# Kernel tuning notes

Measured on AMD Instinct MI355X. Metric: run time of the kernel, lower is better.

The kernel has to match this reference:

```python
import jax, jax.numpy as jnp
import numpy as np

N = 50000
E = 800000
H = 4
D = 64
NEG_SLOPE = 0.2


def gat_conv(h, W, al, ar, b, src, dst):
    # DGL GATConv (eval mode, no dropout): Wh = h @ W -> [N,H,D]
    Wh = (h @ W).reshape(N, H, D)
    el = jnp.sum(Wh * al[None], axis=-1)  # [N,H]
    er = jnp.sum(Wh * ar[None], axis=-1)  # [N,H]
    e = el[src] + er[dst]                 # [E,H]
    e = jnp.where(e > 0, e, NEG_SLOPE * e)  # leaky_relu
    # edge softmax per destination node
    m = jax.lax.stop_gradient(jax.ops.segment_max(e, dst, num_segments=N))
    m = jnp.where(jnp.isfinite(m), m, 0.0)
    ex = jnp.exp(e - m[dst])              # [E,H]
    s = jax.ops.segment_sum(ex, dst, num_segments=N)
    alpha = ex / s[dst]                   # [E,H]
    msg = Wh[src] * alpha[:, :, None]     # [E,H,D]
    out = jax.ops.segment_sum(msg, dst, num_segments=N)  # [N,H,D]
    out = out + b.reshape(1, H, D)
    out = jax.nn.elu(out)                 # activation=F.elu
    return out.reshape(N, H * D)


def setup_inputs() -> dict:
    key = jax.random.key(0)
    ks = jax.random.split(key, 16)
    inp = {
        "h": jax.random.normal(ks[0], (N, 256), dtype=jnp.float32),
        "src0": jax.random.randint(ks[1], (E,), 0, N, dtype=jnp.int32),
        "dst0": jax.random.randint(ks[2], (E,), 0, N, dtype=jnp.int32),
        "src1": jax.random.randint(ks[3], (E,), 0, N, dtype=jnp.int32),
        "dst1": jax.random.randint(ks[4], (E,), 0, N, dtype=jnp.int32),
        "W0": jax.random.normal(ks[5], (256, H * D), dtype=jnp.float32) * 0.05,
        "al0": jax.random.normal(ks[6], (H, D), dtype=jnp.float32) * 0.05,
        "ar0": jax.random.normal(ks[7], (H, D), dtype=jnp.float32) * 0.05,
        "b0": jnp.zeros((H * D,), dtype=jnp.float32),
        "W1": jax.random.normal(ks[8], (256, H * D), dtype=jnp.float32) * 0.05,
        "al1": jax.random.normal(ks[9], (H, D), dtype=jnp.float32) * 0.05,
        "ar1": jax.random.normal(ks[10], (H, D), dtype=jnp.float32) * 0.05,
        "b1": jnp.zeros((H * D,), dtype=jnp.float32),
        "Wp1": jax.random.normal(ks[11], (H * D, 128), dtype=jnp.float32) * 0.05,
        "bp1": jnp.zeros((128,), dtype=jnp.float32),
        "Wp2": jax.random.normal(ks[12], (128, 1), dtype=jnp.float32) * 0.05,
    }
    return inp


def reference(h, src0, dst0, src1, dst1, W0, al0, ar0, b0, W1, al1, ar1, b1, Wp1, bp1, Wp2):
    z0 = gat_conv(h, W0, al0, ar0, b0, src0, dst0)  # [N, H*D]
    z1 = gat_conv(h, W1, al1, ar1, b1, src1, dst1)  # [N, H*D]
    z = jnp.stack([z0, z1], axis=1)                 # [N, P=2, H*D]
    # SemanticAttention: Linear -> tanh -> Linear(no bias) -> softmax over meta-paths
    w = jnp.tanh(z @ Wp1 + bp1) @ Wp2               # [N, P, 1]
    beta = jax.nn.softmax(w[..., 0], axis=1)        # [N, P]
    return jnp.sum(beta[:, :, None] * z, axis=1)    # [N, H*D]
```

## Files before the change

kernel.cpp:

```cpp
#include <hip/hip_runtime.h>
#include <math.h>

#define NN 50000
#define NE 800000
#define NH 4
#define ND 64
#define NF 256
#define NEG_SLOPE 0.2f

typedef __attribute__((ext_vector_type(8))) short s16x8;
typedef __attribute__((ext_vector_type(4))) float f32x4;

__device__ __forceinline__ float elu1(float x) { return x > 0.f ? x : (__expf(x) - 1.f); }
__device__ __forceinline__ float lrelu(float x) { return x > 0.f ? x : NEG_SLOPE * x; }

__device__ __forceinline__ unsigned short f2b(float x) {
    unsigned int u = __float_as_uint(x);
    u = (u + 0x7FFFu + ((u >> 16) & 1u)) >> 16;
    return (unsigned short)u;
}
__device__ __forceinline__ float blo(unsigned int u) { return __uint_as_float(u << 16); }
__device__ __forceinline__ float bhi(unsigned int u) { return __uint_as_float(u & 0xFFFF0000u); }
__device__ __forceinline__ float sel4(float a0, float a1, float a2, float a3, int h) {
    float r = a0;
    r = (h == 1) ? a1 : r;
    r = (h == 2) ? a2 : r;
    r = (h == 3) ? a3 : r;
    return r;
}

__global__ __launch_bounds__(256) void prep(const float* __restrict__ W0,
                                            const float* __restrict__ W1,
                                            const float* __restrict__ Wp1,
                                            short* __restrict__ WT0,
                                            short* __restrict__ WT1,
                                            short* __restrict__ Wp1T) {
    int t = threadIdx.x, b = blockIdx.x, job = blockIdx.y;
    if (job < 2) {
        const float* W = job ? W1 : W0;
        short* WT = job ? WT1 : WT0;
        WT[b * 256 + t] = (short)f2b(W[t * 256 + b]);
    } else if (b < 128) {
        Wp1T[b * 256 + t] = (short)f2b(Wp1[t * 128 + b]);
    }
}

__global__ __launch_bounds__(256) void gemm_mfma(const float* __restrict__ A,
                                                 const short* __restrict__ WTb,
                                                 const float* __restrict__ al,
                                                 const float* __restrict__ ar,
                                                 unsigned short* __restrict__ Whb,
                                                 float* __restrict__ el,
                                                 float* __restrict__ er) {
    int t = threadIdx.x;
    int hh = t >> 6;
    int l = t & 63;
    int r16 = l & 15, kq = l >> 4;
    int m0 = blockIdx.x * 16;

    f32x4 acc[4] = {{0,0,0,0},{0,0,0,0},{0,0,0,0},{0,0,0,0}};
    const float* arow = A + (size_t)(m0 + r16) * 256;
    const short* bbase = WTb + (size_t)hh * 64 * 256;

    #pragma unroll
    for (int k0 = 0; k0 < 256; k0 += 32) {
        float4 f0 = *(const float4*)(arow + k0 + kq * 8);
        float4 f1 = *(const float4*)(arow + k0 + kq * 8 + 4);
        s16x8 af;
        af[0] = (short)f2b(f0.x); af[1] = (short)f2b(f0.y);
        af[2] = (short)f2b(f0.z); af[3] = (short)f2b(f0.w);
        af[4] = (short)f2b(f1.x); af[5] = (short)f2b(f1.y);
        af[6] = (short)f2b(f1.z); af[7] = (short)f2b(f1.w);
        #pragma unroll
        for (int nt = 0; nt < 4; ++nt) {
            s16x8 bf = *(const s16x8*)(bbase + (size_t)(nt * 16 + r16) * 256 + k0 + kq * 8);
            acc[nt] = __builtin_amdgcn_mfma_f32_16x16x32_bf16(af, bf, acc[nt], 0, 0, 0);
        }
    }

    float elp[4] = {0,0,0,0}, erp[4] = {0,0,0,0};
    #pragma unroll
    for (int nt = 0; nt < 4; ++nt) {
        int col = nt * 16 + r16;
        float alv = al[hh * 64 + col];
        float arv = ar[hh * 64 + col];
        #pragma unroll
        for (int r = 0; r < 4; ++r) {
            float v = acc[nt][r];
            int row = m0 + kq * 4 + r;
            Whb[(size_t)row * 256 + hh * 64 + col] = f2b(v);
            elp[r] += v * alv;
            erp[r] += v * arv;
        }
    }
    #pragma unroll
    for (int msk = 1; msk < 16; msk <<= 1) {
        #pragma unroll
        for (int r = 0; r < 4; ++r) {
            elp[r] += __shfl_xor(elp[r], msk);
            erp[r] += __shfl_xor(erp[r], msk);
        }
    }
    if (r16 == 0) {
        #pragma unroll
        for (int r = 0; r < 4; ++r) {
            int row = m0 + kq * 4 + r;
            el[row * 4 + hh] = elp[r];
            er[row * 4 + hh] = erp[r];
        }
    }
}

__global__ __launch_bounds__(256) void hist_kernel(const int* __restrict__ dst, int* __restrict__ deg) {
    int e = blockIdx.x * 256 + threadIdx.x;
    if (e < NE) atomicAdd(&deg[dst[e]], 1);
}

__global__ __launch_bounds__(256) void scan_blk(const int* __restrict__ deg,
                                                int* __restrict__ rp,
                                                int* __restrict__ bsum) {
    __shared__ int ls[256];
    int b = blockIdx.x, t = threadIdx.x;
    int base = b * 1024 + t * 4;
    int v0 = (base + 0 < NN) ? deg[base + 0] : 0;
    int v1 = (base + 1 < NN) ? deg[base + 1] : 0;
    int v2 = (base + 2 < NN) ? deg[base + 2] : 0;
    int v3 = (base + 3 < NN) ? deg[base + 3] : 0;
    int p0 = v0, p1 = p0 + v1, p2 = p1 + v2, p3 = p2 + v3;
    ls[t] = p3;
    __syncthreads();
    int x = p3;
    #pragma unroll
    for (int off = 1; off < 256; off <<= 1) {
        int add = (t >= off) ? ls[t - off] : 0;
        __syncthreads();
        x += add;
        ls[t] = x;
        __syncthreads();
    }
    int excl = x - p3;
    if (base + 0 < NN) rp[base + 0] = excl;
    if (base + 1 < NN) rp[base + 1] = excl + p0;
    if (base + 2 < NN) rp[base + 2] = excl + p1;
    if (base + 3 < NN) rp[base + 3] = excl + p2;
    if (t == 255) bsum[b] = x;
}

__global__ __launch_bounds__(64) void scan_tops(int* __restrict__ bsum, int* __restrict__ rp, int nblk) {
    int t = threadIdx.x;
    int orig = (t < nblk) ? bsum[t] : 0;
    int v = orig;
    #pragma unroll
    for (int off = 1; off < 64; off <<= 1) {
        int y = __shfl_up(v, off);
        if (t >= off) v += y;
    }
    bsum[t] = v - orig;
    int total = __shfl(v, nblk - 1);
    if (t == 0) rp[NN] = total;
}

__global__ __launch_bounds__(256) void scan_add(int* __restrict__ rp,
                                                const int* __restrict__ bsum,
                                                int* __restrict__ cur) {
    int i = blockIdx.x * 256 + threadIdx.x;
    if (i < NN) {
        int v = rp[i] + bsum[i >> 10];
        rp[i] = v;
        cur[i] = v;
    }
}

__global__ __launch_bounds__(256) void fill_kernel(const int* __restrict__ src,
                                                   const int* __restrict__ dst,
                                                   int* __restrict__ cur,
                                                   int* __restrict__ colv) {
    int e = blockIdx.x * 256 + threadIdx.x;
    if (e < NE) {
        int pos = atomicAdd(&cur[dst[e]], 1);
        colv[pos] = src[e];
    }
}

__global__ __launch_bounds__(512) void node_agg(const int* __restrict__ rp,
                                                const int* __restrict__ colv,
                                                const float* __restrict__ el,
                                                const float* __restrict__ er,
                                                const unsigned short* __restrict__ Whb,
                                                const float* __restrict__ bias,
                                                unsigned short* __restrict__ zb,
                                                int path) {
    int t = threadIdx.x;
    int wid = t >> 6;
    int lane = t & 63;
    int n = blockIdx.x * 8 + wid;
    int beg = rp[n], end = rp[n + 1];
    float4 erv = *(const float4*)&er[(size_t)n * 4];

    int eg = lane >> 4, sl = lane & 15;
    int h = sl >> 2;
    float er_h = sel4(erv.x, erv.y, erv.z, erv.w, h);
    float acc[16];
    #pragma unroll
    for (int i = 0; i < 16; ++i) acc[i] = 0.f;
    float s = 0.f;

    for (int j0 = beg; j0 < end; j0 += 4) {
        int j = j0 + eg;
        bool act = j < end;
        int sidx = colv[act ? j : beg];
        float e_l = el[(size_t)sidx * 4 + h];
        float p = act ? __expf(lrelu(e_l + er_h)) : 0.f;
        s += p;
        const unsigned short* wr = &Whb[(size_t)sidx * 256 + sl * 16];
        uint4 u0 = *(const uint4*)wr;
        uint4 u1 = *(const uint4*)(wr + 8);
        acc[0]  += p * blo(u0.x); acc[1]  += p * bhi(u0.x);
        acc[2]  += p * blo(u0.y); acc[3]  += p * bhi(u0.y);
        acc[4]  += p * blo(u0.z); acc[5]  += p * bhi(u0.z);
        acc[6]  += p * blo(u0.w); acc[7]  += p * bhi(u0.w);
        acc[8]  += p * blo(u1.x); acc[9]  += p * bhi(u1.x);
        acc[10] += p * blo(u1.y); acc[11] += p * bhi(u1.y);
        acc[12] += p * blo(u1.z); acc[13] += p * bhi(u1.z);
        acc[14] += p * blo(u1.w); acc[15] += p * bhi(u1.w);
    }
    #pragma unroll
    for (int i = 0; i < 16; ++i) {
        acc[i] += __shfl_xor(acc[i], 16);
        acc[i] += __shfl_xor(acc[i], 32);
    }
    s += __shfl_xor(s, 16);
    s += __shfl_xor(s, 32);

    if (lane < 16) {
        float inv = (s > 0.f) ? 1.f / s : 0.f;
        unsigned int pk[8];
        #pragma unroll
        for (int i = 0; i < 8; ++i) {
            float za = elu1(acc[2 * i] * inv + bias[sl * 16 + 2 * i]);
            float zbv = elu1(acc[2 * i + 1] * inv + bias[sl * 16 + 2 * i + 1]);
            pk[i] = (unsigned int)f2b(za) | ((unsigned int)f2b(zbv) << 16);
        }
        unsigned int* op = (unsigned int*)(zb + (size_t)n * 512 + path * 256 + sl * 16);
        uint4 o0 = {pk[0], pk[1], pk[2], pk[3]};
        uint4 o1 = {pk[4], pk[5], pk[6], pk[7]};
        *(uint4*)op = o0;
        *(uint4*)(op + 4) = o1;
    }
}

__global__ __launch_bounds__(256) void semantic_mfma(const unsigned short* __restrict__ zb,
                                                     const short* __restrict__ Wp1T,
                                                     const float* __restrict__ bp1,
                                                     const float* __restrict__ Wp2,
                                                     float* __restrict__ w) {
    int t = threadIdx.x;
    int gw = blockIdx.x * 4 + (t >> 6);
    if (gw >= 6250) return;
    int l = t & 63;
    int r16 = l & 15, kq = l >> 4;
    int row0 = gw * 16;
    int path = (row0 >= NN) ? 1 : 0;
    int rbase = path ? row0 - NN : row0;
    const unsigned short* arow = zb + (size_t)(rbase + r16) * 512 + path * 256;

    f32x4 acc[8] = {{0,0,0,0},{0,0,0,0},{0,0,0,0},{0,0,0,0},
                    {0,0,0,0},{0,0,0,0},{0,0,0,0},{0,0,0,0}};
    #pragma unroll
    for (int k0 = 0; k0 < 256; k0 += 32) {
        s16x8 af = *(const s16x8*)(arow + k0 + kq * 8);
        #pragma unroll
        for (int nt = 0; nt < 8; ++nt) {
            s16x8 bf = *(const s16x8*)(Wp1T + (size_t)(nt * 16 + r16) * 256 + k0 + kq * 8);
            acc[nt] = __builtin_amdgcn_mfma_f32_16x16x32_bf16(af, bf, acc[nt], 0, 0, 0);
        }
    }
    float wpart[4] = {0,0,0,0};
    #pragma unroll
    for (int nt = 0; nt < 8; ++nt) {
        int col = nt * 16 + r16;
        float bpv = bp1[col], wpv = Wp2[col];
        #pragma unroll
        for (int r = 0; r < 4; ++r) wpart[r] += tanhf(acc[nt][r] + bpv) * wpv;
    }
    #pragma unroll
    for (int msk = 1; msk < 16; msk <<= 1) {
        #pragma unroll
        for (int r = 0; r < 4; ++r) wpart[r] += __shfl_xor(wpart[r], msk);
    }
    if (r16 == 0) {
        #pragma unroll
        for (int r = 0; r < 4; ++r) w[row0 + kq * 4 + r] = wpart[r];
    }
}

__global__ __launch_bounds__(256) void combine(float* __restrict__ zio,
                                               const float* __restrict__ w) {
    int n = blockIdx.x * 4 + (threadIdx.x >> 6);
    int c = (threadIdx.x & 63) * 4;
    const unsigned short* z0p = (const unsigned short*)zio + (size_t)n * 512 + c;
    uint2 u0 = *(const uint2*)z0p;
    uint2 u1 = *(const uint2*)(z0p + 256);
    float w0v = w[n], w1v = w[n + NN];
    __syncthreads();
    float mw = fmaxf(w0v, w1v);
    float e0 = __expf(w0v - mw), e1 = __expf(w1v - mw);
    float inv = 1.f / (e0 + e1);
    float b0 = e0 * inv, b1 = e1 * inv;
    float4 o;
    o.x = b0 * blo(u0.x) + b1 * blo(u1.x);
    o.y = b0 * bhi(u0.x) + b1 * bhi(u1.x);
    o.z = b0 * blo(u0.y) + b1 * blo(u1.y);
    o.w = b0 * bhi(u0.y) + b1 * bhi(u1.y);
    *(float4*)&zio[(size_t)n * 256 + c] = o;
}

extern "C" void kernel_launch(void* const* d_in, const int* in_sizes, int n_in,
                              void* d_out, int out_size, void* d_ws, size_t ws_size,
                              hipStream_t stream) {
    const float* h   = (const float*)d_in[0];
    const int* src0  = (const int*)d_in[1];
    const int* dst0  = (const int*)d_in[2];
    const int* src1  = (const int*)d_in[3];
    const int* dst1  = (const int*)d_in[4];
    const float* W0  = (const float*)d_in[5];
    const float* al0 = (const float*)d_in[6];
    const float* ar0 = (const float*)d_in[7];
    const float* b0  = (const float*)d_in[8];
    const float* W1  = (const float*)d_in[9];
    const float* al1 = (const float*)d_in[10];
    const float* ar1 = (const float*)d_in[11];
    const float* b1  = (const float*)d_in[12];
    const float* Wp1 = (const float*)d_in[13];
    const float* bp1 = (const float*)d_in[14];
    const float* Wp2 = (const float*)d_in[15];

    unsigned short* Whb = (unsigned short*)d_ws;
    float* el  = (float*)(Whb + (size_t)NN * NF);
    float* er  = el + (size_t)NN * NH;
    float* w   = er + (size_t)NN * NH;
    int*   deg = (int*)(w + 2 * NN);
    int*   rp  = deg + NN;
    int*   cur = rp + NN + 1;
    int*   colv = cur + NN;
    int*   bsum = colv + NE;
    short* WT0 = (short*)(bsum + 64);
    short* WT1 = WT0 + 256 * 256;
    short* Wp1T = WT1 + 256 * 256;
    unsigned short* zb = (unsigned short*)d_out;

    const int NBLK = (NN + 1023) / 1024;

    prep<<<dim3(256, 3), 256, 0, stream>>>(W0, W1, Wp1, WT0, WT1, Wp1T);

    for (int p = 0; p < 2; ++p) {
        const int* src  = p ? src1 : src0;
        const int* dst  = p ? dst1 : dst0;
        const float* al = p ? al1 : al0;
        const float* ar = p ? ar1 : ar0;
        const float* bb = p ? b1 : b0;
        const short* WT = p ? WT1 : WT0;

        hipMemsetAsync(deg, 0, NN * sizeof(int), stream);
        hist_kernel<<<(NE + 255) / 256, 256, 0, stream>>>(dst, deg);
        scan_blk<<<NBLK, 256, 0, stream>>>(deg, rp, bsum);
        scan_tops<<<1, 64, 0, stream>>>(bsum, rp, NBLK);
        scan_add<<<(NN + 255) / 256, 256, 0, stream>>>(rp, bsum, cur);
        fill_kernel<<<(NE + 255) / 256, 256, 0, stream>>>(src, dst, cur, colv);
        gemm_mfma<<<NN / 16, 256, 0, stream>>>(h, WT, al, ar, Whb, el, er);
        node_agg<<<NN / 8, 512, 0, stream>>>(rp, colv, el, er, Whb, bb, zb, p);
    }
    semantic_mfma<<<(6250 + 3) / 4, 256, 0, stream>>>(zb, Wp1T, bp1, Wp2, w);
    combine<<<NN / 4, 256, 0, stream>>>((float*)d_out, w);
}
```

Measured before the change: 685.8 us.

## Tile GEMM over 64 rows per block and stage bf16 output through shared memory

Each block of the projection GEMM now covers 64 rows instead of 16, so every B-fragment load feeds four MFMA row tiles and W traffic drops. Results are written through a padded LDS tile so each lane does 16-byte coalesced stores of bf16 Wh rather than scattered 2-byte writes. The cost is many more accumulator registers per thread (64 floats of acc plus el/er partials), which may reduce occupancy. The grid is four times smaller, and bounds checks handle the tail.

```diff
diff --git a/kernel.cpp b/kernel.cpp
--- a/kernel.cpp
+++ b/kernel.cpp
@@ -52,62 +52,108 @@
                                                  unsigned short* __restrict__ Whb,
                                                  float* __restrict__ el,
                                                  float* __restrict__ er) {
+    __shared__ unsigned short st[4][16][72];
     int t = threadIdx.x;
     int hh = t >> 6;
     int l = t & 63;
     int r16 = l & 15, kq = l >> 4;
-    int m0 = blockIdx.x * 16;
-
-    f32x4 acc[4] = {{0,0,0,0},{0,0,0,0},{0,0,0,0},{0,0,0,0}};
-    const float* arow = A + (size_t)(m0 + r16) * 256;
+    int m0 = blockIdx.x * 64;
+
+    f32x4 acc[4][4];
+    #pragma unroll
+    for (int mt = 0; mt < 4; ++mt)
+        #pragma unroll
+        for (int nt = 0; nt < 4; ++nt)
+            acc[mt][nt] = (f32x4){0.f, 0.f, 0.f, 0.f};
+
     const short* bbase = WTb + (size_t)hh * 64 * 256;
+    const float* arow[4];
+    #pragma unroll
+    for (int mt = 0; mt < 4; ++mt) {
+        int row = m0 + mt * 16 + r16;
+        if (row > NN - 1) row = NN - 1;
+        arow[mt] = A + (size_t)row * 256;
+    }
 
     #pragma unroll
     for (int k0 = 0; k0 < 256; k0 += 32) {
-        float4 f0 = *(const float4*)(arow + k0 + kq * 8);
-        float4 f1 = *(const float4*)(arow + k0 + kq * 8 + 4);
-        s16x8 af;
-        af[0] = (short)f2b(f0.x); af[1] = (short)f2b(f0.y);
-        af[2] = (short)f2b(f0.z); af[3] = (short)f2b(f0.w);
-        af[4] = (short)f2b(f1.x); af[5] = (short)f2b(f1.y);
-        af[6] = (short)f2b(f1.z); af[7] = (short)f2b(f1.w);
-        #pragma unroll
-        for (int nt = 0; nt < 4; ++nt) {
-            s16x8 bf = *(const s16x8*)(bbase + (size_t)(nt * 16 + r16) * 256 + k0 + kq * 8);
-            acc[nt] = __builtin_amdgcn_mfma_f32_16x16x32_bf16(af, bf, acc[nt], 0, 0, 0);
+        s16x8 bf[4];
+        #pragma unroll
+        for (int nt = 0; nt < 4; ++nt)
+            bf[nt] = *(const s16x8*)(bbase + (size_t)(nt * 16 + r16) * 256 + k0 + kq * 8);
+        #pragma unroll
+        for (int mt = 0; mt < 4; ++mt) {
+            float4 f0 = *(const float4*)(arow[mt] + k0 + kq * 8);
+            float4 f1 = *(const float4*)(arow[mt] + k0 + kq * 8 + 4);
+            s16x8 af;
+            af[0] = (short)f2b(f0.x); af[1] = (short)f2b(f0.y);
+            af[2] = (short)f2b(f0.z); af[3] = (short)f2b(f0.w);
+            af[4] = (short)f2b(f1.x); af[5] = (short)f2b(f1.y);
+            af[6] = (short)f2b(f1.z); af[7] = (short)f2b(f1.w);
+            #pragma unroll
+            for (int nt = 0; nt < 4; ++nt)
+                acc[mt][nt] = __builtin_amdgcn_mfma_f32_16x16x32_bf16(af, bf[nt], acc[mt][nt], 0, 0, 0);
         }
     }
 
-    float elp[4] = {0,0,0,0}, erp[4] = {0,0,0,0};
+    float elp[4][4], erp[4][4];
+    #pragma unroll
+    for (int mt = 0; mt < 4; ++mt)
+        #pragma unroll
+        for (int r = 0; r < 4; ++r) { elp[mt][r] = 0.f; erp[mt][r] = 0.f; }
     #pragma unroll
     for (int nt = 0; nt < 4; ++nt) {
-        int col = nt * 16 + r16;
-        float alv = al[hh * 64 + col];
-        float arv = ar[hh * 64 + col];
-        #pragma unroll
-        for (int r = 0; r < 4; ++r) {
-            float v = acc[nt][r];
-            int row = m0 + kq * 4 + r;
-            Whb[(size_t)row * 256 + hh * 64 + col] = f2b(v);
-            elp[r] += v * alv;
-            erp[r] += v * arv;
+        float alv = al[hh * 64 + nt * 16 + r16];
+        float arv = ar[hh * 64 + nt * 16 + r16];
+        #pragma unroll
+        for (int mt = 0; mt < 4; ++mt)
+            #pragma unroll
+            for (int r = 0; r < 4; ++r) {
+                float v = acc[mt][nt][r];
+                elp[mt][r] += v * alv;
+                erp[mt][r] += v * arv;
+            }
+    }
+    #pragma unroll
+    for (int msk = 1; msk < 16; msk <<= 1)
+        #pragma unroll
+        for (int mt = 0; mt < 4; ++mt)
+            #pragma unroll
+            for (int r = 0; r < 4; ++r) {
+                elp[mt][r] += __shfl_xor(elp[mt][r], msk);
+                erp[mt][r] += __shfl_xor(erp[mt][r], msk);
+            }
+
+    int srow = l >> 3;
+    int chunk = l & 7;
+    #pragma unroll
+    for (int mt = 0; mt < 4; ++mt) {
+        #pragma unroll
+        for (int nt = 0; nt < 4; ++nt)
+            #pragma unroll
+            for (int r = 0; r < 4; ++r)
+                st[hh][kq * 4 + r][nt * 16 + r16] = f2b(acc[mt][nt][r]);
+        #pragma unroll
+        for (int half = 0; half < 2; ++half) {
+            int rr = srow + half * 8;
+            int grow = m0 + mt * 16 + rr;
+            uint4 v = *(const uint4*)&st[hh][rr][chunk * 8];
+            if (grow < NN)
+                *(uint4*)&Whb[(size_t)grow * 256 + hh * 64 + chunk * 8] = v;
         }
     }
-    #pragma unroll
-    for (int msk = 1; msk < 16; msk <<= 1) {
-        #pragma unroll
-        for (int r = 0; r < 4; ++r) {
-            elp[r] += __shfl_xor(elp[r], msk);
-            erp[r] += __shfl_xor(erp[r], msk);
-        }
-    }
+
     if (r16 == 0) {
         #pragma unroll
-        for (int r = 0; r < 4; ++r) {
-            int row = m0 + kq * 4 + r;
-            el[row * 4 + hh] = elp[r];
-            er[row * 4 + hh] = erp[r];
-        }
+        for (int mt = 0; mt < 4; ++mt)
+            #pragma unroll
+            for (int r = 0; r < 4; ++r) {
+                int row = m0 + mt * 16 + kq * 4 + r;
+                if (row < NN) {
+                    el[row * 4 + hh] = elp[mt][r];
+                    er[row * 4 + hh] = erp[mt][r];
+                }
+            }
     }
 }
 
@@ -367,7 +413,7 @@
         scan_tops<<<1, 64, 0, stream>>>(bsum, rp, NBLK);
         scan_add<<<(NN + 255) / 256, 256, 0, stream>>>(rp, bsum, cur);
         fill_kernel<<<(NE + 255) / 256, 256, 0, stream>>>(src, dst, cur, colv);
-        gemm_mfma<<<NN / 16, 256, 0, stream>>>(h, WT, al, ar, Whb, el, er);
+        gemm_mfma<<<(NN + 63) / 64, 256, 0, stream>>>(h, WT, al, ar, Whb, el, er);
         node_agg<<<NN / 8, 512, 0, stream>>>(rp, colv, el, er, Whb, bb, zb, p);
     }
     semantic_mfma<<<(6250 + 3) / 4, 256, 0, stream>>>(zb, Wp1T, bp1, Wp2, w);
```

New measurement: 635.3 us. 7.4% less time.
